# Performance work log

Hardware: AMD Instinct MI355X
Metric: run time of the kernel (lower is better)

Reference implementation:

```python
import jax, jax.numpy as jnp
import numpy as np

B, F, NUM_LAYERS, T, DEPTH, C = 256, 128, 4, 2048, 6, 100
L = 2 ** DEPTH  # num_leaves = 64

# bit pattern of the oblivious tree: bit d of leaf_idx (MSB-first),
# matching (leaf_idx // (L >> (d+1))) % 2 in the original double loop
_BITS = np.stack([(np.arange(L) // (L >> (d + 1))) % 2 for d in range(DEPTH)])  # [DEPTH, L]


def setup_inputs() -> dict:
    key = jax.random.key(0)
    k = jax.random.split(key, 5)
    x = jax.random.normal(k[0], (B, F), dtype=jnp.float32)
    sel_W = jax.random.normal(k[1], (NUM_LAYERS, T * DEPTH, F), dtype=jnp.float32) * 0.05
    sel_b = jax.random.normal(k[2], (NUM_LAYERS, T * DEPTH), dtype=jnp.float32) * 0.01
    out_W = jax.random.normal(k[3], (C, NUM_LAYERS * T * L), dtype=jnp.float32) * 0.002
    out_b = jax.random.normal(k[4], (C,), dtype=jnp.float32) * 0.01
    return {"x": x, "sel_W": sel_W, "sel_b": sel_b, "out_W": out_W, "out_b": out_b}


def reference(x, sel_W, sel_b, out_W, out_b):
    bits = jnp.asarray(_BITS, dtype=x.dtype)  # [DEPTH, L]
    layer_outputs = []
    for i in range(NUM_LAYERS):
        # feature selector linear -> [B, T, DEPTH] threshold responses
        fv = jax.nn.sigmoid(x @ sel_W[i].T + sel_b[i]).reshape(B, T, DEPTH)
        # leaf probability = prod over depth of (left or right prob per bit)
        leaf = jnp.ones((B, T, L), dtype=x.dtype)
        for d in range(DEPTH):  # fixed small structural loop (depth=6)
            p = fv[:, :, d:d + 1]                     # [B, T, 1] left prob
            bit = bits[d]                             # [L]
            leaf = leaf * (p * (1.0 - bit) + (1.0 - p) * bit)
        layer_outputs.append(leaf.reshape(B, T * L))
    combined = jnp.concatenate(layer_outputs, axis=1)  # [B, NUM_LAYERS*T*L]
    return combined @ out_W.T + out_b
```

## Files before the change

kernel.cpp:

```cpp
#include <hip/hip_runtime.h>

#define BB 256
#define FF 128
#define CC 100
#define KG 512
#define ITPB 16

typedef short bf16x8 __attribute__((ext_vector_type(8)));
typedef float f32x4 __attribute__((ext_vector_type(4)));

#define LDS_BARRIER() asm volatile("s_waitcnt lgkmcnt(0)\n\ts_barrier" ::: "memory")

static __device__ inline unsigned short f2bf(float f) {
    unsigned u = __float_as_uint(f);
    u += 0x7fffu + ((u >> 16) & 1u);
    return (unsigned short)(u >> 16);
}
static __device__ inline float bf2f(unsigned short h) {
    return __uint_as_float(((unsigned)h) << 16);
}

__global__ __launch_bounds__(256) void fv_kernel(
    const float* __restrict__ x, const float* __restrict__ selW,
    const float* __restrict__ selb, unsigned short* __restrict__ fvout)
{
    __shared__ unsigned short wt[128 * 136];
    __shared__ unsigned short xt[128 * 136];
    __shared__ float sb[128];

    const int tid = threadIdx.x;
    const int m0 = blockIdx.x * 128;
    const int n0 = blockIdx.y * 128;

    #pragma unroll 4
    for (int pass = 0; pass < 16; ++pass) {
        int idx = pass * 256 + tid;
        int r = idx >> 5, f4 = idx & 31;
        float4 v = *((const float4*)(selW + (size_t)(m0 + r) * FF) + f4);
        ushort4 h;
        h.x = f2bf(v.x); h.y = f2bf(v.y); h.z = f2bf(v.z); h.w = f2bf(v.w);
        *(ushort4*)(wt + r * 136 + f4 * 4) = h;
        float4 vx = *((const float4*)(x + (size_t)(n0 + r) * FF) + f4);
        ushort4 hx;
        hx.x = f2bf(vx.x); hx.y = f2bf(vx.y); hx.z = f2bf(vx.z); hx.w = f2bf(vx.w);
        *(ushort4*)(xt + r * 136 + f4 * 4) = hx;
    }
    if (tid < 128) sb[tid] = selb[m0 + tid];
    __syncthreads();

    const int w = tid >> 6, lane = tid & 63;
    const int q = lane >> 4, l15 = lane & 15;
    const int mq = w & 1, nq = w >> 1;

    f32x4 zero4 = {0.f, 0.f, 0.f, 0.f};
    f32x4 acc[4][4];
    #pragma unroll
    for (int i = 0; i < 4; ++i)
        #pragma unroll
        for (int j = 0; j < 4; ++j) acc[i][j] = zero4;

    #pragma unroll
    for (int ch = 0; ch < 4; ++ch) {
        bf16x8 a[4];
        #pragma unroll
        for (int ms = 0; ms < 4; ++ms)
            a[ms] = *(const bf16x8*)(wt + (mq * 64 + ms * 16 + l15) * 136 + ch * 32 + q * 8);
        #pragma unroll
        for (int ns = 0; ns < 4; ++ns) {
            bf16x8 bfr = *(const bf16x8*)(xt + (nq * 64 + ns * 16 + l15) * 136 + ch * 32 + q * 8);
            #pragma unroll
            for (int ms = 0; ms < 4; ++ms)
                acc[ms][ns] = __builtin_amdgcn_mfma_f32_16x16x32_bf16(a[ms], bfr, acc[ms][ns], 0, 0, 0);
        }
    }

    #pragma unroll
    for (int ms = 0; ms < 4; ++ms) {
        int rowl = mq * 64 + ms * 16 + q * 4;
        #pragma unroll
        for (int ns = 0; ns < 4; ++ns) {
            int b = n0 + nq * 64 + ns * 16 + l15;
            #pragma unroll
            for (int reg = 0; reg < 4; ++reg) {
                int row = m0 + rowl + reg;
                float z = acc[ms][ns][reg] + sb[rowl + reg];
                float p = 1.0f / (1.0f + __expf(-z));
                fvout[(size_t)row * 256 + b] = f2bf(p);
            }
        }
    }
}

__global__ __launch_bounds__(256, 2) void main_gemm(
    const unsigned short* __restrict__ fv, const float* __restrict__ outW,
    float* __restrict__ part)
{
    __shared__ unsigned short leaf[256 * 72];
    __shared__ unsigned short wt[112 * 72];

    const int tid = threadIdx.x;
    const int kg = blockIdx.x;
    const int w = tid >> 6, lane = tid & 63;
    const int q = lane >> 4, l15 = lane & 15;
    const int cc = tid >> 4, f4 = tid & 15;

    f32x4 zero4 = {0.f, 0.f, 0.f, 0.f};
    f32x4 acc[4][7];
    #pragma unroll
    for (int i = 0; i < 4; ++i)
        #pragma unroll
        for (int j = 0; j < 7; ++j) acc[i][j] = zero4;

    float4 wv[7];
    unsigned short pv[6];
    {
        const int it = kg * ITPB;
        #pragma unroll
        for (int pass = 0; pass < 7; ++pass) {
            const int c = pass * 16 + cc;
            float4 v = make_float4(0.f, 0.f, 0.f, 0.f);
            if (c < CC)
                v = *((const float4*)(outW + (size_t)c * 524288 + (size_t)it * 64) + f4);
            wv[pass] = v;
        }
        const unsigned short* fp = fv + (size_t)it * 1536 + tid;
        #pragma unroll
        for (int d = 0; d < 6; ++d) pv[d] = fp[d * 256];
    }

    for (int itl = 0; itl < ITPB; ++itl) {
        LDS_BARRIER();

        #pragma unroll
        for (int pass = 0; pass < 7; ++pass) {
            const int c = pass * 16 + cc;
            ushort4 h;
            h.x = f2bf(wv[pass].x); h.y = f2bf(wv[pass].y);
            h.z = f2bf(wv[pass].z); h.w = f2bf(wv[pass].w);
            *(ushort4*)(wt + c * 72 + f4 * 4) = h;
        }

        {
            float p0 = bf2f(pv[0]), p1 = bf2f(pv[1]), p2 = bf2f(pv[2]);
            float p3 = bf2f(pv[3]), p4 = bf2f(pv[4]), p5 = bf2f(pv[5]);
            float q0 = 1.f - p0, q1 = 1.f - p1, q2 = 1.f - p2;
            float q3 = 1.f - p3, q4 = 1.f - p4, q5 = 1.f - p5;
            float A[4]  = {p0 * p1, p0 * q1, q0 * p1, q0 * q1};
            float B2[4] = {p2 * p3, p2 * q3, q2 * p3, q2 * q3};
            float C2[4] = {p4 * p5, p4 * q5, q4 * p5, q4 * q5};
            float BC[16];
            #pragma unroll
            for (int m = 0; m < 16; ++m) BC[m] = B2[m >> 2] * C2[m & 3];
            unsigned short* row = leaf + tid * 72;
            #pragma unroll
            for (int j = 0; j < 8; ++j) {
                uint4 dw;
                unsigned int* dwp = (unsigned int*)&dw;
                #pragma unroll
                for (int e = 0; e < 4; ++e) {
                    int l0 = j * 8 + 2 * e;
                    float v0 = A[l0 >> 4] * BC[l0 & 15];
                    float v1 = A[(l0 + 1) >> 4] * BC[(l0 + 1) & 15];
                    dwp[e] = (unsigned)f2bf(v0) | ((unsigned)f2bf(v1) << 16);
                }
                *(uint4*)(row + j * 8) = dw;
            }
        }

        {
            const int itn = kg * ITPB + ((itl + 1) & (ITPB - 1));
            #pragma unroll
            for (int pass = 0; pass < 7; ++pass) {
                const int c = pass * 16 + cc;
                if (c < CC)
                    wv[pass] = *((const float4*)(outW + (size_t)c * 524288 + (size_t)itn * 64) + f4);
            }
            const unsigned short* fp = fv + (size_t)itn * 1536 + tid;
            #pragma unroll
            for (int d = 0; d < 6; ++d) pv[d] = fp[d * 256];
        }

        LDS_BARRIER();

        #pragma unroll
        for (int ch = 0; ch < 2; ++ch) {
            bf16x8 a[4];
            #pragma unroll
            for (int ms = 0; ms < 4; ++ms)
                a[ms] = *(const bf16x8*)(leaf + (w * 64 + ms * 16 + l15) * 72 + ch * 32 + q * 8);
            #pragma unroll
            for (int nt = 0; nt < 7; ++nt) {
                bf16x8 bb = *(const bf16x8*)(wt + (nt * 16 + l15) * 72 + ch * 32 + q * 8);
                #pragma unroll
                for (int ms = 0; ms < 4; ++ms)
                    acc[ms][nt] = __builtin_amdgcn_mfma_f32_16x16x32_bf16(a[ms], bb, acc[ms][nt], 0, 0, 0);
            }
        }
    }

    #pragma unroll
    for (int ms = 0; ms < 4; ++ms) {
        const int brow = w * 64 + ms * 16 + q * 4;
        #pragma unroll
        for (int nt = 0; nt < 7; ++nt) {
            const int c = nt * 16 + l15;
            #pragma unroll
            for (int reg = 0; reg < 4; ++reg)
                part[((size_t)(brow + reg) * KG + kg) * 112 + c] = acc[ms][nt][reg];
        }
    }
}

__global__ __launch_bounds__(256) void reduce_k(
    const float* __restrict__ part, const float* __restrict__ outb,
    float* __restrict__ out)
{
    __shared__ float red[9 * 112];
    const int b = blockIdx.x;
    const int tid = threadIdx.x;
    const float* slice = part + (size_t)b * (KG * 112);

    if (tid < 252) {
        const int kgsub = tid / 28;
        const int c4 = tid - kgsub * 28;
        f32x4 s = {0.f, 0.f, 0.f, 0.f};
        #pragma unroll 8
        for (int i = 0; i < 56; ++i) {
            f32x4 v = *((const f32x4*)slice + (i * 252 + tid));
            s += v;
        }
        if (kgsub < 8) {
            f32x4 v = *((const f32x4*)slice + ((504 + kgsub) * 28 + c4));
            s += v;
        }
        *(f32x4*)(red + kgsub * 112 + c4 * 4) = s;
    }
    __syncthreads();
    if (tid < CC) {
        float r = outb[tid];
        #pragma unroll
        for (int k = 0; k < 9; ++k) r += red[k * 112 + tid];
        out[b * CC + tid] = r;
    }
}

extern "C" void kernel_launch(void* const* d_in, const int* in_sizes, int n_in,
                              void* d_out, int out_size, void* d_ws, size_t ws_size,
                              hipStream_t stream) {
    const float* x    = (const float*)d_in[0];
    const float* selW = (const float*)d_in[1];
    const float* selb = (const float*)d_in[2];
    const float* outW = (const float*)d_in[3];
    const float* outb = (const float*)d_in[4];
    float* out = (float*)d_out;

    unsigned short* fv = (unsigned short*)d_ws;
    float* part = (float*)((char*)d_ws + 25165824);

    fv_kernel<<<dim3(384, 2), 256, 0, stream>>>(x, selW, selb, fv);
    main_gemm<<<KG, 256, 0, stream>>>(fv, outW, part);
    reduce_k<<<BB, 256, 0, stream>>>(part, outb, out);
}
```

Before: 355.5 us.

## Store split-K partials in fp16, double-buffer prefetch, reorder fv loads

Partial sums from the main GEMM are now written as fp16 instead of fp32, which halves the partial-buffer write and the read in the reduction kernel. The reduction is rewritten to load 8-wide fp16 vectors and accumulate in fp32. The main loop's register prefetch becomes two-deep, so loads for iteration i+2 are issued while iteration i is processed. In fv_kernel the x load is issued earlier. fp16 partials lose some precision and add register pressure.

```diff
diff --git a/kernel.cpp b/kernel.cpp
--- a/kernel.cpp
+++ b/kernel.cpp
@@ -8,6 +8,7 @@
 
 typedef short bf16x8 __attribute__((ext_vector_type(8)));
 typedef float f32x4 __attribute__((ext_vector_type(4)));
+typedef _Float16 f16x8 __attribute__((ext_vector_type(8)));
 
 #define LDS_BARRIER() asm volatile("s_waitcnt lgkmcnt(0)\n\ts_barrier" ::: "memory")
 
@@ -37,10 +38,10 @@
         int idx = pass * 256 + tid;
         int r = idx >> 5, f4 = idx & 31;
         float4 v = *((const float4*)(selW + (size_t)(m0 + r) * FF) + f4);
+        float4 vx = *((const float4*)(x + (size_t)(n0 + r) * FF) + f4);
         ushort4 h;
         h.x = f2bf(v.x); h.y = f2bf(v.y); h.z = f2bf(v.z); h.w = f2bf(v.w);
         *(ushort4*)(wt + r * 136 + f4 * 4) = h;
-        float4 vx = *((const float4*)(x + (size_t)(n0 + r) * FF) + f4);
         ushort4 hx;
         hx.x = f2bf(vx.x); hx.y = f2bf(vx.y); hx.z = f2bf(vx.z); hx.w = f2bf(vx.w);
         *(ushort4*)(xt + r * 136 + f4 * 4) = hx;
@@ -93,7 +94,7 @@
 
 __global__ __launch_bounds__(256, 2) void main_gemm(
     const unsigned short* __restrict__ fv, const float* __restrict__ outW,
-    float* __restrict__ part)
+    _Float16* __restrict__ part16)
 {
     __shared__ unsigned short leaf[256 * 72];
     __shared__ unsigned short wt[112 * 72];
@@ -111,38 +112,41 @@
         #pragma unroll
         for (int j = 0; j < 7; ++j) acc[i][j] = zero4;
 
-    float4 wv[7];
-    unsigned short pv[6];
-    {
-        const int it = kg * ITPB;
+    float4 wv[2][7];
+    unsigned short pv[2][6];
+    #pragma unroll
+    for (int pb = 0; pb < 2; ++pb) {
+        const int it = kg * ITPB + pb;
         #pragma unroll
         for (int pass = 0; pass < 7; ++pass) {
             const int c = pass * 16 + cc;
             float4 v = make_float4(0.f, 0.f, 0.f, 0.f);
             if (c < CC)
                 v = *((const float4*)(outW + (size_t)c * 524288 + (size_t)it * 64) + f4);
-            wv[pass] = v;
+            wv[pb][pass] = v;
         }
         const unsigned short* fp = fv + (size_t)it * 1536 + tid;
         #pragma unroll
-        for (int d = 0; d < 6; ++d) pv[d] = fp[d * 256];
-    }
-
+        for (int d = 0; d < 6; ++d) pv[pb][d] = fp[d * 256];
+    }
+
+    #pragma unroll 2
     for (int itl = 0; itl < ITPB; ++itl) {
+        const int cur = itl & 1;
         LDS_BARRIER();
 
         #pragma unroll
         for (int pass = 0; pass < 7; ++pass) {
             const int c = pass * 16 + cc;
             ushort4 h;
-            h.x = f2bf(wv[pass].x); h.y = f2bf(wv[pass].y);
-            h.z = f2bf(wv[pass].z); h.w = f2bf(wv[pass].w);
+            h.x = f2bf(wv[cur][pass].x); h.y = f2bf(wv[cur][pass].y);
+            h.z = f2bf(wv[cur][pass].z); h.w = f2bf(wv[cur][pass].w);
             *(ushort4*)(wt + c * 72 + f4 * 4) = h;
         }
 
         {
-            float p0 = bf2f(pv[0]), p1 = bf2f(pv[1]), p2 = bf2f(pv[2]);
-            float p3 = bf2f(pv[3]), p4 = bf2f(pv[4]), p5 = bf2f(pv[5]);
+            float p0 = bf2f(pv[cur][0]), p1 = bf2f(pv[cur][1]), p2 = bf2f(pv[cur][2]);
+            float p3 = bf2f(pv[cur][3]), p4 = bf2f(pv[cur][4]), p5 = bf2f(pv[cur][5]);
             float q0 = 1.f - p0, q1 = 1.f - p1, q2 = 1.f - p2;
             float q3 = 1.f - p3, q4 = 1.f - p4, q5 = 1.f - p5;
             float A[4]  = {p0 * p1, p0 * q1, q0 * p1, q0 * q1};
@@ -168,16 +172,16 @@
         }
 
         {
-            const int itn = kg * ITPB + ((itl + 1) & (ITPB - 1));
+            const int itn = kg * ITPB + ((itl + 2) & (ITPB - 1));
             #pragma unroll
             for (int pass = 0; pass < 7; ++pass) {
                 const int c = pass * 16 + cc;
                 if (c < CC)
-                    wv[pass] = *((const float4*)(outW + (size_t)c * 524288 + (size_t)itn * 64) + f4);
+                    wv[cur][pass] = *((const float4*)(outW + (size_t)c * 524288 + (size_t)itn * 64) + f4);
             }
             const unsigned short* fp = fv + (size_t)itn * 1536 + tid;
             #pragma unroll
-            for (int d = 0; d < 6; ++d) pv[d] = fp[d * 256];
+            for (int d = 0; d < 6; ++d) pv[cur][d] = fp[d * 256];
         }
 
         LDS_BARRIER();
@@ -206,40 +210,41 @@
             const int c = nt * 16 + l15;
             #pragma unroll
             for (int reg = 0; reg < 4; ++reg)
-                part[((size_t)(brow + reg) * KG + kg) * 112 + c] = acc[ms][nt][reg];
+                part16[((size_t)(brow + reg) * KG + kg) * 112 + c] =
+                    (_Float16)acc[ms][nt][reg];
         }
     }
 }
 
 __global__ __launch_bounds__(256) void reduce_k(
-    const float* __restrict__ part, const float* __restrict__ outb,
+    const _Float16* __restrict__ part16, const float* __restrict__ outb,
     float* __restrict__ out)
 {
-    __shared__ float red[9 * 112];
+    __shared__ float red[16 * 112];
     const int b = blockIdx.x;
     const int tid = threadIdx.x;
-    const float* slice = part + (size_t)b * (KG * 112);
-
-    if (tid < 252) {
-        const int kgsub = tid / 28;
-        const int c4 = tid - kgsub * 28;
-        f32x4 s = {0.f, 0.f, 0.f, 0.f};
-        #pragma unroll 8
-        for (int i = 0; i < 56; ++i) {
-            f32x4 v = *((const f32x4*)slice + (i * 252 + tid));
-            s += v;
-        }
-        if (kgsub < 8) {
-            f32x4 v = *((const f32x4*)slice + ((504 + kgsub) * 28 + c4));
-            s += v;
-        }
-        *(f32x4*)(red + kgsub * 112 + c4 * 4) = s;
+    const f16x8* slice = (const f16x8*)(part16 + (size_t)b * (KG * 112));
+
+    if (tid < 224) {
+        const int c8 = tid % 14;
+        const int kgs = tid / 14;
+        float s[8];
+        #pragma unroll
+        for (int j = 0; j < 8; ++j) s[j] = 0.f;
+        #pragma unroll 4
+        for (int i = 0; i < 32; ++i) {
+            f16x8 v = slice[i * 224 + tid];
+            #pragma unroll
+            for (int j = 0; j < 8; ++j) s[j] += (float)v[j];
+        }
+        #pragma unroll
+        for (int j = 0; j < 8; ++j) red[kgs * 112 + c8 * 8 + j] = s[j];
     }
     __syncthreads();
     if (tid < CC) {
         float r = outb[tid];
         #pragma unroll
-        for (int k = 0; k < 9; ++k) r += red[k * 112 + tid];
+        for (int k = 0; k < 16; ++k) r += red[k * 112 + tid];
         out[b * CC + tid] = r;
     }
 }
@@ -255,9 +260,9 @@
     float* out = (float*)d_out;
 
     unsigned short* fv = (unsigned short*)d_ws;
-    float* part = (float*)((char*)d_ws + 25165824);
+    _Float16* part16 = (_Float16*)((char*)d_ws + 25165824);
 
     fv_kernel<<<dim3(384, 2), 256, 0, stream>>>(x, selW, selb, fv);
-    main_gemm<<<KG, 256, 0, stream>>>(fv, outW, part);
-    reduce_k<<<BB, 256, 0, stream>>>(part, outb, out);
-}
+    main_gemm<<<KG, 256, 0, stream>>>(fv, outW, part16);
+    reduce_k<<<BB, 256, 0, stream>>>(part16, outb, out);
+}
```

Result: slower. 374.9 us (+5.5%).
